# Kernel tuning notes

Measured on AMD Instinct MI355X. Metric: run time of the kernel, lower is better.

Reference implementation:

```python
import jax, jax.numpy as jnp
import numpy as np

RWKV_K_CLAMP = 60.0
B, T, C = 8, 1024, 1024
LAYER_ID, N_LAYER = 2, 12


def _decay_speed():
    # replicate RWKV_TimeMix.__init__ decay_speed construction
    first = 1
    f1 = 3.0 + (LAYER_ID - first) / (N_LAYER - 1 - first) * (1.2 - 3.0)
    f2 = 0.65 + (LAYER_ID - first) / (N_LAYER - 1 - first) * (0.4 - 0.65)
    if LAYER_ID == first:
        f1 += 0.5
    if LAYER_ID == N_LAYER - 2:
        f2 = 0.4
    if LAYER_ID == N_LAYER - 1:
        f2 = 0.37
    h = np.arange(C, dtype=np.float64)
    return (f2 ** (h / (C - 1) * 7.0)) * f1


def setup_inputs() -> dict:
    key = jax.random.key(0)
    ks = jax.random.split(key, 6)
    scale = 1.0 / np.sqrt(C)
    time_mix = np.ones((C,), np.float32)
    time_mix[: C // 2] = 0.0
    return {
        "x": jax.random.normal(ks[0], (B, T, C), jnp.float32),
        "time_decay": jnp.asarray(np.log(_decay_speed()), jnp.float32),  # (C,)
        "time_first": jnp.full((C,), np.log(0.3), jnp.float32),
        "time_mix": jnp.asarray(time_mix),
        "combined_mix": jnp.full((C,), 0.01, jnp.float32),
        "Wk": jax.random.normal(ks[1], (C, C), jnp.float32) * scale,
        "Wv": jax.random.normal(ks[2], (C, C), jnp.float32) * scale,
        "Wr": jax.random.normal(ks[3], (C, C), jnp.float32) * scale,
        "Wo": jax.random.normal(ks[4], (C, C), jnp.float32) * scale,
    }


def _wkv(w, u, k, v):
    # w,u: (C,); k,v: (B,T,C). Numerically-stable decayed linear recurrence
    # (RWKV wkv kernel: running-max, like online softmax).
    b = k.shape[0]
    init = (
        jnp.zeros((b, C), k.dtype),            # numerator state a
        jnp.zeros((b, C), k.dtype),            # denominator state b
        jnp.full((b, C), -1e38, k.dtype),      # running max exponent p
    )

    def step(carry, kv):
        a, bb, p = carry
        kt, vt = kv  # (B,C)
        no = jnp.maximum(p, u + kt)
        e1 = jnp.exp(p - no)
        e2 = jnp.exp(u + kt - no)
        y = (e1 * a + e2 * vt) / (e1 * bb + e2)
        no2 = jnp.maximum(w + p, kt)
        e1 = jnp.exp(w + p - no2)
        e2 = jnp.exp(kt - no2)
        return (e1 * a + e2 * vt, e1 * bb + e2, no2), y

    _, y = jax.lax.scan(step, init, (k.transpose(1, 0, 2), v.transpose(1, 0, 2)))
    return y.transpose(1, 0, 2)  # (B,T,C)


def reference(x, time_decay, time_first, time_mix, combined_mix, Wk, Wv, Wr, Wo):
    b, t, c = x.shape
    zrow = jnp.zeros((b, 1, c), x.dtype)
    x_m1 = jnp.concatenate([zrow, x[:, :-1, :]], axis=1)   # time_shift / x_{t-1}
    x_p1 = jnp.concatenate([x[:, 1:, :], zrow], axis=1)    # x_{t+1}
    half = c // 2
    x_comb = jnp.concatenate([x_m1[:, :, :half], x_p1[:, :, half:]], axis=-1)
    xm = x * time_mix + x_m1 * (1.0 - time_mix) + x_comb * combined_mix
    k = jnp.exp(jnp.minimum(jnp.einsum("btc,dc->btd", xm, Wk), RWKV_K_CLAMP))
    v = jnp.einsum("btc,dc->btd", xm, Wv)
    r = jnp.einsum("btc,dc->btd", xm, Wr)
    wkv = _wkv(time_decay / t, time_first / t, k, v)
    return jnp.einsum("btc,dc->btd", jax.nn.sigmoid(r) * wkv, Wo)
```

## Files before the change

kernel.cpp:

```cpp
#include <hip/hip_runtime.h>
#include <hip/hip_bf16.h>
#include <stdint.h>

#define B_SZ 8
#define T_LEN 1024
#define C_DIM 1024
#define M_ROWS (B_SZ * T_LEN)
#define NCH 32
#define CHL (T_LEN / NCH)

typedef unsigned short ushort_t;
typedef __attribute__((ext_vector_type(8))) short short8;
typedef __attribute__((ext_vector_type(4))) float f32x4;
typedef __attribute__((ext_vector_type(4))) unsigned short us4;

static __device__ __forceinline__ float bf2f(ushort_t u) {
  union { unsigned int i; float f; } x; x.i = ((unsigned int)u) << 16; return x.f;
}
static __device__ __forceinline__ ushort_t f2bf(float f) {
  union { float f; unsigned int i; } x; x.f = f;
  unsigned int r = x.i + 0x7fffu + ((x.i >> 16) & 1u);
  return (ushort_t)(r >> 16);
}

static __device__ __forceinline__ void gload_lds16(const void* g, void* l) {
  __builtin_amdgcn_global_load_lds(
      (const __attribute__((address_space(1))) void*)g,
      (__attribute__((address_space(3))) void*)l, 16, 0, 0);
}

__global__ void cvt_w_kernel(const float* __restrict__ wk, const float* __restrict__ wv,
                             const float* __restrict__ wr, const float* __restrict__ wo,
                             ushort_t* __restrict__ out) {
  int gid = blockIdx.x * 256 + threadIdx.x;
  int which = gid >> 18;
  int off = (gid << 2) & ((1 << 20) - 1);
  const float* src = which == 0 ? wk : which == 1 ? wv : which == 2 ? wr : wo;
  float4 v = *(const float4*)(src + off);
  us4 o = {f2bf(v.x), f2bf(v.y), f2bf(v.z), f2bf(v.w)};
  *(us4*)(out + (size_t)gid * 4) = o;
}

__global__ void xm_kernel(const float* __restrict__ x, const float* __restrict__ tm,
                          const float* __restrict__ cm, ushort_t* __restrict__ xmb) {
  int gid = blockIdx.x * 256 + threadIdx.x;
  int c4 = (gid & (C_DIM / 4 - 1)) * 4;
  int t = (gid >> 8) & (T_LEN - 1);
  const float4 zero = {0.f, 0.f, 0.f, 0.f};
  float4 xv = *(const float4*)(x + (size_t)gid * 4);
  float4 xp = (t > 0) ? *(const float4*)(x + (size_t)gid * 4 - C_DIM) : zero;
  float4 xn = (t < T_LEN - 1) ? *(const float4*)(x + (size_t)gid * 4 + C_DIM) : zero;
  float4 tmv = *(const float4*)(tm + c4);
  float4 cmv = *(const float4*)(cm + c4);
  float4 xc = (c4 < C_DIM / 2) ? xp : xn;
  us4 o;
  o.x = f2bf(xv.x * tmv.x + xp.x * (1.f - tmv.x) + xc.x * cmv.x);
  o.y = f2bf(xv.y * tmv.y + xp.y * (1.f - tmv.y) + xc.y * cmv.y);
  o.z = f2bf(xv.z * tmv.z + xp.z * (1.f - tmv.z) + xc.z * cmv.z);
  o.w = f2bf(xv.w * tmv.w + xp.w * (1.f - tmv.w) + xc.w * cmv.w);
  *(us4*)(xmb + (size_t)gid * 4) = o;
}

template <int FUSED>
__global__ __launch_bounds__(256) void gemm_bt(const ushort_t* __restrict__ A,
                                               const ushort_t* __restrict__ Bw,
                                               float* __restrict__ outF,
                                               ushort_t* __restrict__ outV,
                                               ushort_t* __restrict__ outR) {
  constexpr int K = 1024;
  constexpr int NT = K / 32;
  __shared__ ushort_t As[2][128 * 32];
  __shared__ ushort_t Bs[2][128 * 32];

  const int tid = threadIdx.x;
  const int lane = tid & 63;
  const int wave = tid >> 6;

  const int bid = blockIdx.x;
  const int xcd = bid & 7;
  const int r = bid >> 3;
  const int bm = (xcd * 8 + (r & 7)) * 128;
  const int jb = r >> 3;
  const int mode = FUSED ? (jb >> 3) : 3;
  const int bn = FUSED ? (jb & 7) * 128 : jb * 128;
  const ushort_t* Bp = FUSED ? (Bw + ((size_t)(jb >> 3) << 20)) : Bw;

  const int wr = (wave >> 1) * 64;
  const int wc = (wave & 1) * 64;

  f32x4 acc[4][4];
#pragma unroll
  for (int m = 0; m < 4; ++m)
#pragma unroll
    for (int n = 0; n < 4; ++n) acc[m][n] = (f32x4){0.f, 0.f, 0.f, 0.f};

  const int srow = tid >> 2;
  const int scol = (((tid & 3) ^ ((srow >> 1) & 3)) * 8);
  const ushort_t* Ag = A + (size_t)(bm + srow) * K + scol;
  const ushort_t* Bg = Bp + (size_t)(bn + srow) * K + scol;
  ushort_t* AsP0 = &As[0][tid * 8];
  ushort_t* BsP0 = &Bs[0][tid * 8];
  ushort_t* AsP1 = &As[1][tid * 8];
  ushort_t* BsP1 = &Bs[1][tid * 8];

  const int fr = lane & 15;
  const int kq = lane >> 4;
  const int ps = (kq ^ ((fr >> 1) & 3)) * 8;

  auto stage = [&](int buf, int k0) {
    ushort_t* ap = buf ? AsP1 : AsP0;
    ushort_t* bp = buf ? BsP1 : BsP0;
    gload_lds16(Ag + k0, ap);
    gload_lds16(Ag + (size_t)64 * K + k0, ap + 64 * 32);
    gload_lds16(Bg + k0, bp);
    gload_lds16(Bg + (size_t)64 * K + k0, bp + 64 * 32);
  };

  stage(0, 0);
  asm volatile("s_waitcnt vmcnt(0)" ::: "memory");
  __syncthreads();

  int cur = 0;
  for (int t = 0; t < NT; ++t) {
    if (t < NT - 1) stage(cur ^ 1, (t + 1) * 32);
    short8 af[4], bfr[4];
#pragma unroll
    for (int m = 0; m < 4; ++m)
      af[m] = *(const short8*)&As[cur][(wr + m * 16 + fr) * 32 + ps];
#pragma unroll
    for (int n = 0; n < 4; ++n)
      bfr[n] = *(const short8*)&Bs[cur][(wc + n * 16 + fr) * 32 + ps];
#pragma unroll
    for (int m = 0; m < 4; ++m)
#pragma unroll
      for (int n = 0; n < 4; ++n)
        acc[m][n] = __builtin_amdgcn_mfma_f32_16x16x32_bf16(af[m], bfr[n], acc[m][n], 0, 0, 0);
    asm volatile("s_waitcnt vmcnt(0)" ::: "memory");
    __syncthreads();
    cur ^= 1;
  }

  const int crow0 = (lane >> 4) * 4;
#pragma unroll
  for (int m = 0; m < 4; ++m)
#pragma unroll
    for (int n = 0; n < 4; ++n)
#pragma unroll
      for (int j = 0; j < 4; ++j) {
        float v = acc[m][n][j];
        size_t idx = (size_t)(bm + wr + m * 16 + crow0 + j) * C_DIM + (bn + wc + n * 16 + fr);
        if (mode == 0) {
          outF[idx] = __expf(fminf(v, 60.f));
        } else if (mode == 1) {
          outV[idx] = f2bf(v);
        } else if (mode == 2) {
          outR[idx] = f2bf(1.f / (1.f + __expf(-v)));
        } else {
          outF[idx] = v;
        }
      }
}

__global__ void wkv_phaseA(const float* __restrict__ kk, const ushort_t* __restrict__ vv,
                           const float* __restrict__ td,
                           float* __restrict__ sa, float* __restrict__ sb,
                           float* __restrict__ sp) {
  int gid = blockIdx.x * 256 + threadIdx.x;
  int c = gid & (C_DIM - 1);
  int ch = (gid >> 10) & (NCH - 1);
  int b = gid >> 15;
  float w = td[c] * (1.f / T_LEN);
  size_t base = ((size_t)b * T_LEN + ch * CHL) * C_DIM + c;
  float a = 0.f, bb = 0.f, p = -1e38f;
  for (int t = 0; t < CHL; ++t) {
    float kt = kk[base + (size_t)t * C_DIM];
    float vt = bf2f(vv[base + (size_t)t * C_DIM]);
    float no2 = fmaxf(w + p, kt);
    float e1 = __expf(w + p - no2);
    float e2 = __expf(kt - no2);
    a = e1 * a + e2 * vt;
    bb = e1 * bb + e2;
    p = no2;
  }
  sa[gid] = a; sb[gid] = bb; sp[gid] = p;
}

__global__ void wkv_phaseC2(const float* __restrict__ kk, const ushort_t* __restrict__ vv,
                            const ushort_t* __restrict__ sr, const float* __restrict__ td,
                            const float* __restrict__ tf,
                            const float* __restrict__ sa, const float* __restrict__ sb,
                            const float* __restrict__ sp, ushort_t* __restrict__ sy) {
  int gid = blockIdx.x * 256 + threadIdx.x;
  int c = gid & (C_DIM - 1);
  int ch = (gid >> 10) & (NCH - 1);
  int b = gid >> 15;
  float w = td[c] * (1.f / T_LEN);
  float u = tf[c] * (1.f / T_LEN);
  float wL = w * (float)CHL;

  float a = 0.f, bb = 0.f, p = -1e38f;
  size_t sbase = ((size_t)b * NCH) * C_DIM + c;
  for (int j = 0; j < ch; ++j) {
    float ac = sa[sbase + (size_t)j * C_DIM];
    float bc = sb[sbase + (size_t)j * C_DIM];
    float pc = sp[sbase + (size_t)j * C_DIM];
    float pn = fmaxf(p + wL, pc);
    float e1 = __expf(p + wL - pn);
    float e2 = __expf(pc - pn);
    a = e1 * a + e2 * ac;
    bb = e1 * bb + e2 * bc;
    p = pn;
  }

  size_t base = ((size_t)b * T_LEN + ch * CHL) * C_DIM + c;
  for (int t = 0; t < CHL; ++t) {
    float kt = kk[base + (size_t)t * C_DIM];
    float vt = bf2f(vv[base + (size_t)t * C_DIM]);
    float no = fmaxf(p, u + kt);
    float e1 = __expf(p - no);
    float e2 = __expf(u + kt - no);
    float y = (e1 * a + e2 * vt) / (e1 * bb + e2);
    float srv = bf2f(sr[base + (size_t)t * C_DIM]);
    sy[base + (size_t)t * C_DIM] = f2bf(srv * y);
    float no2 = fmaxf(w + p, kt);
    e1 = __expf(w + p - no2);
    e2 = __expf(kt - no2);
    a = e1 * a + e2 * vt;
    bb = e1 * bb + e2;
    p = no2;
  }
}

extern "C" void kernel_launch(void* const* d_in, const int* in_sizes, int n_in,
                              void* d_out, int out_size, void* d_ws, size_t ws_size,
                              hipStream_t stream) {
  const float* x  = (const float*)d_in[0];
  const float* td = (const float*)d_in[1];
  const float* tf = (const float*)d_in[2];
  const float* tm = (const float*)d_in[3];
  const float* cm = (const float*)d_in[4];
  const float* Wk = (const float*)d_in[5];
  const float* Wv = (const float*)d_in[6];
  const float* Wr = (const float*)d_in[7];
  const float* Wo = (const float*)d_in[8];

  const size_t MC = (size_t)M_ROWS * C_DIM;
  const size_t CC = (size_t)C_DIM * C_DIM;

  char* ws = (char*)d_ws;
  ushort_t* xmb = (ushort_t*)ws; ws += MC * 2;
  ushort_t* Wb  = (ushort_t*)ws; ws += 4 * CC * 2;
  float*    kk  = (float*)ws;    ws += MC * 4;
  ushort_t* vv  = (ushort_t*)ws; ws += MC * 2;
  ushort_t* sr  = (ushort_t*)ws; ws += MC * 2;
  ushort_t* sy  = (ushort_t*)ws; ws += MC * 2;
  float* sa = (float*)ws; ws += (size_t)B_SZ * NCH * C_DIM * 4;
  float* sb = (float*)ws; ws += (size_t)B_SZ * NCH * C_DIM * 4;
  float* sp = (float*)ws; ws += (size_t)B_SZ * NCH * C_DIM * 4;

  cvt_w_kernel<<<(4 * CC / 4) / 256, 256, 0, stream>>>(Wk, Wv, Wr, Wo, Wb);
  xm_kernel<<<(MC / 4) / 256, 256, 0, stream>>>(x, tm, cm, xmb);

  gemm_bt<1><<<dim3(1536), 256, 0, stream>>>(xmb, Wb, kk, vv, sr);

  wkv_phaseA<<<(B_SZ * NCH * C_DIM) / 256, 256, 0, stream>>>(kk, vv, td, sa, sb, sp);
  wkv_phaseC2<<<(B_SZ * NCH * C_DIM) / 256, 256, 0, stream>>>(kk, vv, sr, td, tf, sa, sb, sp, sy);

  gemm_bt<0><<<dim3(512), 256, 0, stream>>>(sy, Wb + 3 * CC, (float*)d_out, nullptr, nullptr);
}
```

Measured before the change: 166.0 us.

## Deepen GEMM K-tile to 64, store k in bf16, merge prep kernels

The GEMM now stages a 64-wide K slice per iteration with an 8-way XOR swizzle and issues two MFMAs per fragment pair, halving the number of barrier/wait iterations. The exp(k) output is stored as bf16 instead of fp32, cutting write and read traffic for the WKV phases. The weight conversion and token-mix kernels are merged into one launch. LDS use doubles to 64 KB per block, which may limit occupancy, and bf16 k lowers precision inside the recurrence.

```diff
diff --git a/kernel.cpp b/kernel.cpp
--- a/kernel.cpp
+++ b/kernel.cpp
@@ -29,58 +29,62 @@
       (__attribute__((address_space(3))) void*)l, 16, 0, 0);
 }
 
-__global__ void cvt_w_kernel(const float* __restrict__ wk, const float* __restrict__ wv,
-                             const float* __restrict__ wr, const float* __restrict__ wo,
-                             ushort_t* __restrict__ out) {
-  int gid = blockIdx.x * 256 + threadIdx.x;
-  int which = gid >> 18;
-  int off = (gid << 2) & ((1 << 20) - 1);
-  const float* src = which == 0 ? wk : which == 1 ? wv : which == 2 ? wr : wo;
-  float4 v = *(const float4*)(src + off);
-  us4 o = {f2bf(v.x), f2bf(v.y), f2bf(v.z), f2bf(v.w)};
-  *(us4*)(out + (size_t)gid * 4) = o;
-}
-
-__global__ void xm_kernel(const float* __restrict__ x, const float* __restrict__ tm,
-                          const float* __restrict__ cm, ushort_t* __restrict__ xmb) {
-  int gid = blockIdx.x * 256 + threadIdx.x;
-  int c4 = (gid & (C_DIM / 4 - 1)) * 4;
-  int t = (gid >> 8) & (T_LEN - 1);
-  const float4 zero = {0.f, 0.f, 0.f, 0.f};
-  float4 xv = *(const float4*)(x + (size_t)gid * 4);
-  float4 xp = (t > 0) ? *(const float4*)(x + (size_t)gid * 4 - C_DIM) : zero;
-  float4 xn = (t < T_LEN - 1) ? *(const float4*)(x + (size_t)gid * 4 + C_DIM) : zero;
-  float4 tmv = *(const float4*)(tm + c4);
-  float4 cmv = *(const float4*)(cm + c4);
-  float4 xc = (c4 < C_DIM / 2) ? xp : xn;
-  us4 o;
-  o.x = f2bf(xv.x * tmv.x + xp.x * (1.f - tmv.x) + xc.x * cmv.x);
-  o.y = f2bf(xv.y * tmv.y + xp.y * (1.f - tmv.y) + xc.y * cmv.y);
-  o.z = f2bf(xv.z * tmv.z + xp.z * (1.f - tmv.z) + xc.z * cmv.z);
-  o.w = f2bf(xv.w * tmv.w + xp.w * (1.f - tmv.w) + xc.w * cmv.w);
-  *(us4*)(xmb + (size_t)gid * 4) = o;
+__global__ void prep_kernel(const float* __restrict__ wk, const float* __restrict__ wv,
+                            const float* __restrict__ wr, const float* __restrict__ wo,
+                            ushort_t* __restrict__ wout,
+                            const float* __restrict__ x, const float* __restrict__ tm,
+                            const float* __restrict__ cm, ushort_t* __restrict__ xmb) {
+  if (blockIdx.x < 4096) {
+    int gid = blockIdx.x * 256 + threadIdx.x;
+    int which = gid >> 18;
+    int off = (gid << 2) & ((1 << 20) - 1);
+    const float* src = which == 0 ? wk : which == 1 ? wv : which == 2 ? wr : wo;
+    float4 v = *(const float4*)(src + off);
+    us4 o = {f2bf(v.x), f2bf(v.y), f2bf(v.z), f2bf(v.w)};
+    *(us4*)(wout + (size_t)gid * 4) = o;
+  } else {
+    int gid = (blockIdx.x - 4096) * 256 + threadIdx.x;
+    int c4 = (gid & (C_DIM / 4 - 1)) * 4;
+    int t = (gid >> 8) & (T_LEN - 1);
+    const float4 zero = {0.f, 0.f, 0.f, 0.f};
+    float4 xv = *(const float4*)(x + (size_t)gid * 4);
+    float4 xp = (t > 0) ? *(const float4*)(x + (size_t)gid * 4 - C_DIM) : zero;
+    float4 xn = (t < T_LEN - 1) ? *(const float4*)(x + (size_t)gid * 4 + C_DIM) : zero;
+    float4 tmv = *(const float4*)(tm + c4);
+    float4 cmv = *(const float4*)(cm + c4);
+    float4 xc = (c4 < C_DIM / 2) ? xp : xn;
+    us4 o;
+    o.x = f2bf(xv.x * tmv.x + xp.x * (1.f - tmv.x) + xc.x * cmv.x);
+    o.y = f2bf(xv.y * tmv.y + xp.y * (1.f - tmv.y) + xc.y * cmv.y);
+    o.z = f2bf(xv.z * tmv.z + xp.z * (1.f - tmv.z) + xc.z * cmv.z);
+    o.w = f2bf(xv.w * tmv.w + xp.w * (1.f - tmv.w) + xc.w * cmv.w);
+    *(us4*)(xmb + (size_t)gid * 4) = o;
+  }
 }
 
 template <int FUSED>
-__global__ __launch_bounds__(256) void gemm_bt(const ushort_t* __restrict__ A,
-                                               const ushort_t* __restrict__ Bw,
-                                               float* __restrict__ outF,
-                                               ushort_t* __restrict__ outV,
-                                               ushort_t* __restrict__ outR) {
+__global__ __launch_bounds__(256, 2) void gemm_bk64(const ushort_t* __restrict__ A,
+                                                    const ushort_t* __restrict__ Bw,
+                                                    float* __restrict__ outF,
+                                                    ushort_t* __restrict__ outK,
+                                                    ushort_t* __restrict__ outV,
+                                                    ushort_t* __restrict__ outR) {
   constexpr int K = 1024;
-  constexpr int NT = K / 32;
-  __shared__ ushort_t As[2][128 * 32];
-  __shared__ ushort_t Bs[2][128 * 32];
+  constexpr int NT = K / 64;
+  __shared__ ushort_t As[2][128 * 64];
+  __shared__ ushort_t Bs[2][128 * 64];
 
   const int tid = threadIdx.x;
-  const int lane = tid & 63;
+  const int l = tid & 63;
   const int wave = tid >> 6;
+  const int fr = l & 15;
+  const int kq = l >> 4;
 
   const int bid = blockIdx.x;
   const int xcd = bid & 7;
-  const int r = bid >> 3;
-  const int bm = (xcd * 8 + (r & 7)) * 128;
-  const int jb = r >> 3;
+  const int idx = bid >> 3;
+  const int jb = idx >> 3;
+  const int bm = (xcd * 8 + (idx & 7)) * 128;
   const int mode = FUSED ? (jb >> 3) : 3;
   const int bn = FUSED ? (jb & 7) * 128 : jb * 128;
   const ushort_t* Bp = FUSED ? (Bw + ((size_t)(jb >> 3) << 20)) : Bw;
@@ -94,53 +98,59 @@
 #pragma unroll
     for (int n = 0; n < 4; ++n) acc[m][n] = (f32x4){0.f, 0.f, 0.f, 0.f};
 
-  const int srow = tid >> 2;
-  const int scol = (((tid & 3) ^ ((srow >> 1) & 3)) * 8);
-  const ushort_t* Ag = A + (size_t)(bm + srow) * K + scol;
-  const ushort_t* Bg = Bp + (size_t)(bn + srow) * K + scol;
-  ushort_t* AsP0 = &As[0][tid * 8];
-  ushort_t* BsP0 = &Bs[0][tid * 8];
-  ushort_t* AsP1 = &As[1][tid * 8];
-  ushort_t* BsP1 = &Bs[1][tid * 8];
-
-  const int fr = lane & 15;
-  const int kq = lane >> 4;
-  const int ps = (kq ^ ((fr >> 1) & 3)) * 8;
+  int srow[4], scol[4];
+#pragma unroll
+  for (int j = 0; j < 4; ++j) {
+    int row = wave * 32 + j * 8 + (l >> 3);
+    srow[j] = row;
+    scol[j] = ((l & 7) ^ (row & 7)) * 8;
+  }
+  const ushort_t* AgB = A + (size_t)bm * K;
+  const ushort_t* BgB = Bp + (size_t)bn * K;
+  const int dst0 = wave * 2048 + l * 8;
 
   auto stage = [&](int buf, int k0) {
-    ushort_t* ap = buf ? AsP1 : AsP0;
-    ushort_t* bp = buf ? BsP1 : BsP0;
-    gload_lds16(Ag + k0, ap);
-    gload_lds16(Ag + (size_t)64 * K + k0, ap + 64 * 32);
-    gload_lds16(Bg + k0, bp);
-    gload_lds16(Bg + (size_t)64 * K + k0, bp + 64 * 32);
+#pragma unroll
+    for (int j = 0; j < 4; ++j)
+      gload_lds16(AgB + (size_t)srow[j] * K + scol[j] + k0, &As[buf][dst0 + j * 512]);
+#pragma unroll
+    for (int j = 0; j < 4; ++j)
+      gload_lds16(BgB + (size_t)srow[j] * K + scol[j] + k0, &Bs[buf][dst0 + j * 512]);
   };
 
   stage(0, 0);
   asm volatile("s_waitcnt vmcnt(0)" ::: "memory");
   __syncthreads();
 
+  const int ps0 = ((0 * 4 + kq) ^ (fr & 7)) * 8;
+  const int ps1 = ((1 * 4 + kq) ^ (fr & 7)) * 8;
+
   int cur = 0;
   for (int t = 0; t < NT; ++t) {
-    if (t < NT - 1) stage(cur ^ 1, (t + 1) * 32);
-    short8 af[4], bfr[4];
+    if (t < NT - 1) stage(cur ^ 1, (t + 1) * 64);
+    short8 af[4][2], bfr[4][2];
+#pragma unroll
+    for (int m = 0; m < 4; ++m) {
+      af[m][0] = *(const short8*)&As[cur][(wr + m * 16 + fr) * 64 + ps0];
+      af[m][1] = *(const short8*)&As[cur][(wr + m * 16 + fr) * 64 + ps1];
+    }
+#pragma unroll
+    for (int n = 0; n < 4; ++n) {
+      bfr[n][0] = *(const short8*)&Bs[cur][(wc + n * 16 + fr) * 64 + ps0];
+      bfr[n][1] = *(const short8*)&Bs[cur][(wc + n * 16 + fr) * 64 + ps1];
+    }
 #pragma unroll
     for (int m = 0; m < 4; ++m)
-      af[m] = *(const short8*)&As[cur][(wr + m * 16 + fr) * 32 + ps];
-#pragma unroll
-    for (int n = 0; n < 4; ++n)
-      bfr[n] = *(const short8*)&Bs[cur][(wc + n * 16 + fr) * 32 + ps];
-#pragma unroll
-    for (int m = 0; m < 4; ++m)
 #pragma unroll
       for (int n = 0; n < 4; ++n)
-        acc[m][n] = __builtin_amdgcn_mfma_f32_16x16x32_bf16(af[m], bfr[n], acc[m][n], 0, 0, 0);
+#pragma unroll
+        for (int ks = 0; ks < 2; ++ks)
+          acc[m][n] = __builtin_amdgcn_mfma_f32_16x16x32_bf16(af[m][ks], bfr[n][ks], acc[m][n], 0, 0, 0);
     asm volatile("s_waitcnt vmcnt(0)" ::: "memory");
     __syncthreads();
     cur ^= 1;
   }
 
-  const int crow0 = (lane >> 4) * 4;
 #pragma unroll
   for (int m = 0; m < 4; ++m)
 #pragma unroll
@@ -148,20 +158,20 @@
 #pragma unroll
       for (int j = 0; j < 4; ++j) {
         float v = acc[m][n][j];
-        size_t idx = (size_t)(bm + wr + m * 16 + crow0 + j) * C_DIM + (bn + wc + n * 16 + fr);
+        size_t idx2 = (size_t)(bm + wr + m * 16 + kq * 4 + j) * C_DIM + (bn + wc + n * 16 + fr);
         if (mode == 0) {
-          outF[idx] = __expf(fminf(v, 60.f));
+          outK[idx2] = f2bf(__expf(fminf(v, 60.f)));
         } else if (mode == 1) {
-          outV[idx] = f2bf(v);
+          outV[idx2] = f2bf(v);
         } else if (mode == 2) {
-          outR[idx] = f2bf(1.f / (1.f + __expf(-v)));
+          outR[idx2] = f2bf(1.f / (1.f + __expf(-v)));
         } else {
-          outF[idx] = v;
+          outF[idx2] = v;
         }
       }
 }
 
-__global__ void wkv_phaseA(const float* __restrict__ kk, const ushort_t* __restrict__ vv,
+__global__ void wkv_phaseA(const ushort_t* __restrict__ kk, const ushort_t* __restrict__ vv,
                            const float* __restrict__ td,
                            float* __restrict__ sa, float* __restrict__ sb,
                            float* __restrict__ sp) {
@@ -173,7 +183,7 @@
   size_t base = ((size_t)b * T_LEN + ch * CHL) * C_DIM + c;
   float a = 0.f, bb = 0.f, p = -1e38f;
   for (int t = 0; t < CHL; ++t) {
-    float kt = kk[base + (size_t)t * C_DIM];
+    float kt = bf2f(kk[base + (size_t)t * C_DIM]);
     float vt = bf2f(vv[base + (size_t)t * C_DIM]);
     float no2 = fmaxf(w + p, kt);
     float e1 = __expf(w + p - no2);
@@ -185,7 +195,7 @@
   sa[gid] = a; sb[gid] = bb; sp[gid] = p;
 }
 
-__global__ void wkv_phaseC2(const float* __restrict__ kk, const ushort_t* __restrict__ vv,
+__global__ void wkv_phaseC2(const ushort_t* __restrict__ kk, const ushort_t* __restrict__ vv,
                             const ushort_t* __restrict__ sr, const float* __restrict__ td,
                             const float* __restrict__ tf,
                             const float* __restrict__ sa, const float* __restrict__ sb,
@@ -214,7 +224,7 @@
 
   size_t base = ((size_t)b * T_LEN + ch * CHL) * C_DIM + c;
   for (int t = 0; t < CHL; ++t) {
-    float kt = kk[base + (size_t)t * C_DIM];
+    float kt = bf2f(kk[base + (size_t)t * C_DIM]);
     float vt = bf2f(vv[base + (size_t)t * C_DIM]);
     float no = fmaxf(p, u + kt);
     float e1 = __expf(p - no);
@@ -250,7 +260,7 @@
   char* ws = (char*)d_ws;
   ushort_t* xmb = (ushort_t*)ws; ws += MC * 2;
   ushort_t* Wb  = (ushort_t*)ws; ws += 4 * CC * 2;
-  float*    kk  = (float*)ws;    ws += MC * 4;
+  ushort_t* kk  = (ushort_t*)ws; ws += MC * 2;
   ushort_t* vv  = (ushort_t*)ws; ws += MC * 2;
   ushort_t* sr  = (ushort_t*)ws; ws += MC * 2;
   ushort_t* sy  = (ushort_t*)ws; ws += MC * 2;
@@ -258,13 +268,12 @@
   float* sb = (float*)ws; ws += (size_t)B_SZ * NCH * C_DIM * 4;
   float* sp = (float*)ws; ws += (size_t)B_SZ * NCH * C_DIM * 4;
 
-  cvt_w_kernel<<<(4 * CC / 4) / 256, 256, 0, stream>>>(Wk, Wv, Wr, Wo, Wb);
-  xm_kernel<<<(MC / 4) / 256, 256, 0, stream>>>(x, tm, cm, xmb);
-
-  gemm_bt<1><<<dim3(1536), 256, 0, stream>>>(xmb, Wb, kk, vv, sr);
+  prep_kernel<<<dim3(12288), 256, 0, stream>>>(Wk, Wv, Wr, Wo, Wb, x, tm, cm, xmb);
+
+  gemm_bk64<1><<<dim3(1536), 256, 0, stream>>>(xmb, Wb, nullptr, kk, vv, sr);
 
   wkv_phaseA<<<(B_SZ * NCH * C_DIM) / 256, 256, 0, stream>>>(kk, vv, td, sa, sb, sp);
   wkv_phaseC2<<<(B_SZ * NCH * C_DIM) / 256, 256, 0, stream>>>(kk, vv, sr, td, tf, sa, sb, sp, sy);
 
-  gemm_bt<0><<<dim3(512), 256, 0, stream>>>(sy, Wb + 3 * CC, (float*)d_out, nullptr, nullptr);
-}
+  gemm_bk64<0><<<dim3(512), 256, 0, stream>>>(sy, Wb + 3 * CC, (float*)d_out, nullptr, nullptr, nullptr);
+}
```

After: 168.0 us. No clear change (+1.2%).
